# Optimization experiments

Hardware: AMD Instinct MI355X
Metric: run time of the kernel (lower is better)

The kernel has to match this reference:

```python
import jax, jax.numpy as jnp
import numpy as np

# static multi-level geometry (stride 8/16/32/64 on a 1024x1024 image)
SPATIAL_SHAPES = np.array([[128, 128], [64, 64], [32, 32], [16, 16]], dtype=np.int64)
LEVEL_START = np.array([0, 16384, 20480, 21504], dtype=np.int64)
LEN_IN = 21760
N_HEADS, N_LEVELS, N_POINTS = 8, 4, 4
D_MODEL, D_FFN = 256, 1024
N_BATCH, LEN_Q = 8, 2048
EPS = 1e-5


def layer_norm(x, g, b):
    mu = jnp.mean(x, -1, keepdims=True)
    var = jnp.mean((x - mu) ** 2, -1, keepdims=True)
    return (x - mu) * jax.lax.rsqrt(var + EPS) * g + b


def sample_level(val_l, loc_l, Hl, Wl):
    # val_l: [N, nh, Hl*Wl, dh]; loc_l: [N, nh, Lq, P, 2] normalized to [0,1]
    # bilinear, align_corners=False, zero padding (matches F.grid_sample in MSDeformAttn)
    N, nh, _, dh = val_l.shape
    Lq, P = loc_l.shape[2], loc_l.shape[3]
    x = loc_l[..., 0] * Wl - 0.5
    y = loc_l[..., 1] * Hl - 0.5
    x0 = jnp.floor(x)
    y0 = jnp.floor(y)
    wx = (x - x0)[..., None]
    wy = (y - y0)[..., None]

    def gather(xi, yi):
        valid = (xi >= 0) & (xi < Wl) & (yi >= 0) & (yi < Hl)
        xi_c = jnp.clip(xi, 0, Wl - 1).astype(jnp.int32)
        yi_c = jnp.clip(yi, 0, Hl - 1).astype(jnp.int32)
        idx = (yi_c * Wl + xi_c).reshape(N, nh, Lq * P)
        g = jnp.take_along_axis(val_l, idx[..., None], axis=2).reshape(N, nh, Lq, P, dh)
        return g * valid[..., None].astype(val_l.dtype)

    v00 = gather(x0, y0)
    v01 = gather(x0 + 1, y0)
    v10 = gather(x0, y0 + 1)
    v11 = gather(x0 + 1, y0 + 1)
    return v00 * (1 - wx) * (1 - wy) + v01 * wx * (1 - wy) + v10 * (1 - wx) * wy + v11 * wx * wy


def setup_inputs() -> dict:
    key = jax.random.key(0)
    ks = jax.random.split(key, 16)
    s = 0.02
    inp = {
        'src': jax.random.normal(ks[0], (N_BATCH, LEN_Q, D_MODEL), jnp.float32),
        'pos_embed': jax.random.normal(ks[1], (N_BATCH, LEN_Q, D_MODEL), jnp.float32),
        'memorys': jax.random.normal(ks[2], (N_BATCH, LEN_IN, D_MODEL), jnp.float32),
        'pos_memory': jax.random.normal(ks[3], (N_BATCH, LEN_IN, D_MODEL), jnp.float32),
        'reference_points': jax.random.uniform(ks[4], (N_BATCH, LEN_Q, N_LEVELS, 2), jnp.float32),
        'spatial_shapes': jnp.asarray(SPATIAL_SHAPES),
        'level_start_index': jnp.asarray(LEVEL_START),
        # MSDeformAttn params
        'W_off': jax.random.normal(ks[5], (D_MODEL, N_HEADS * N_LEVELS * N_POINTS * 2), jnp.float32) * s,
        'b_off': jax.random.normal(ks[6], (N_HEADS * N_LEVELS * N_POINTS * 2,), jnp.float32) * s,
        'W_attn': jax.random.normal(ks[7], (D_MODEL, N_HEADS * N_LEVELS * N_POINTS), jnp.float32) * s,
        'b_attn': jnp.zeros((N_HEADS * N_LEVELS * N_POINTS,), jnp.float32),
        'W_val': jax.random.normal(ks[8], (D_MODEL, D_MODEL), jnp.float32) * s,
        'b_val': jnp.zeros((D_MODEL,), jnp.float32),
        'W_out': jax.random.normal(ks[9], (D_MODEL, D_MODEL), jnp.float32) * s,
        'b_out': jnp.zeros((D_MODEL,), jnp.float32),
        # norm1
        'g1': jnp.ones((D_MODEL,), jnp.float32),
        'be1': jnp.zeros((D_MODEL,), jnp.float32),
        # FFN (default: linear -> relu -> linear, residual + LayerNorm)
        'W_ff1': jax.random.normal(ks[10], (D_MODEL, D_FFN), jnp.float32) * s,
        'b_ff1': jnp.zeros((D_FFN,), jnp.float32),
        'W_ff2': jax.random.normal(ks[11], (D_FFN, D_MODEL), jnp.float32) * s,
        'b_ff2': jnp.zeros((D_MODEL,), jnp.float32),
        'g2': jnp.ones((D_MODEL,), jnp.float32),
        'be2': jnp.zeros((D_MODEL,), jnp.float32),
    }
    return inp


def reference(src, pos_embed, memorys, pos_memory, reference_points,
              spatial_shapes, level_start_index,
              W_off, b_off, W_attn, b_attn, W_val, b_val, W_out, b_out,
              g1, be1, W_ff1, b_ff1, W_ff2, b_ff2, g2, be2):
    N, Lq, D = src.shape
    nh, L, P = N_HEADS, N_LEVELS, N_POINTS
    dh = D // nh

    q = src + pos_embed                                   # with_pos_embed(src, pos)
    v = (memorys + pos_memory) @ W_val + b_val            # value_proj: [N, Lin, D]
    v = v.reshape(N, -1, nh, dh).transpose(0, 2, 1, 3)    # [N, nh, Lin, dh]

    off = (q @ W_off + b_off).reshape(N, Lq, nh, L, P, 2)
    attn = (q @ W_attn + b_attn).reshape(N, Lq, nh, L * P)
    attn = jax.nn.softmax(attn, axis=-1).reshape(N, Lq, nh, L, P)

    # offset normalizer is (W, H) per level (static geometry)
    norm = jnp.asarray(SPATIAL_SHAPES[:, ::-1].copy(), dtype=src.dtype)
    loc = reference_points[:, :, None, :, None, :] + off / norm[None, None, None, :, None, :]
    loc = loc.transpose(0, 2, 1, 3, 4, 5)                 # [N, nh, Lq, L, P, 2]
    attn = attn.transpose(0, 2, 1, 3, 4)                  # [N, nh, Lq, L, P]

    out = jnp.zeros((N, nh, Lq, dh), src.dtype)
    for l in range(L):  # small static loop over pyramid levels
        Hl, Wl = int(SPATIAL_SHAPES[l, 0]), int(SPATIAL_SHAPES[l, 1])
        s0 = int(LEVEL_START[l])
        val_l = jax.lax.dynamic_slice_in_dim(v, s0, Hl * Wl, axis=2)
        samp = sample_level(val_l, loc[:, :, :, l], Hl, Wl)   # [N, nh, Lq, P, dh]
        out = out + jnp.einsum('nhqp,nhqpd->nhqd', attn[:, :, :, l], samp)

    out = out.transpose(0, 2, 1, 3).reshape(N, Lq, D)
    src2 = out @ W_out + b_out                            # output_proj
    x = layer_norm(src + src2, g1, be1)                   # add + norm1 (dropout=eval identity)
    h = jax.nn.relu(x @ W_ff1 + b_ff1) @ W_ff2 + b_ff2    # default FFN
    return layer_norm(x + h, g2, be2)
```

## Files before the change

kernel.cpp:

```cpp
#include <hip/hip_runtime.h>
#include <hip/hip_bf16.h>
#include <stdint.h>

typedef __attribute__((ext_vector_type(4))) float f32x4;
typedef __attribute__((ext_vector_type(8))) short bf16x8;
typedef __attribute__((ext_vector_type(8))) unsigned short u16x8;
typedef __attribute__((ext_vector_type(4))) unsigned short u16x4;

#define LEN_Q 2048
#define D_MODEL 256
#define LEN_IN 21760

static __device__ __forceinline__ unsigned short f2bf(float f) {
  unsigned int u = __float_as_uint(f);
  u += 0x7fffu + ((u >> 16) & 1u);
  return (unsigned short)(u >> 16);
}
static __device__ __forceinline__ float bf2f(unsigned int us) {
  return __uint_as_float(us << 16);
}

__global__ __launch_bounds__(256) void prep_k(
    const float* __restrict__ Wv, const float* __restrict__ Wo,
    const float* __restrict__ Wa, const float* __restrict__ Wu,
    const float* __restrict__ W1, const float* __restrict__ W2,
    const float* __restrict__ boff, const float* __restrict__ batt,
    unsigned short* __restrict__ WTv, unsigned short* __restrict__ WToa,
    unsigned short* __restrict__ WTu, unsigned short* __restrict__ WT1,
    unsigned short* __restrict__ WT2, float* __restrict__ b_oa) {
  int i = blockIdx.x * 256 + threadIdx.x;
  if (i < 65536) { int n = i >> 8, k = i & 255; WTv[i] = f2bf(Wv[k * 256 + n]); return; }
  i -= 65536;
  if (i < 65536) { int n = i >> 8, k = i & 255; WToa[i] = f2bf(Wo[k * 256 + n]); return; }
  i -= 65536;
  if (i < 32768) { int n = i >> 8, k = i & 255; WToa[65536 + i] = f2bf(Wa[k * 128 + n]); return; }
  i -= 32768;
  if (i < 65536) { int n = i >> 8, k = i & 255; WTu[i] = f2bf(Wu[k * 256 + n]); return; }
  i -= 65536;
  if (i < 262144) { int n = i >> 8, k = i & 255; WT1[i] = f2bf(W1[k * 1024 + n]); return; }
  i -= 262144;
  if (i < 262144) { int n = i >> 10, k = i & 1023; WT2[i] = f2bf(W2[k * 256 + n]); return; }
  i -= 262144;
  if (i < 256) { b_oa[i] = boff[i]; return; }
  i -= 256;
  if (i < 128) { b_oa[256 + i] = batt[i]; }
}

__global__ __launch_bounds__(256) void addcvt_k(const float* __restrict__ a,
                                                const float* __restrict__ b,
                                                unsigned short* __restrict__ o, int n4) {
  int i = blockIdx.x * 256 + threadIdx.x;
  if (i < n4) {
    f32x4 x = ((const f32x4*)a)[i];
    f32x4 y = ((const f32x4*)b)[i];
    u16x4 r;
#pragma unroll
    for (int j = 0; j < 4; ++j) r[j] = f2bf(x[j] + y[j]);
    ((u16x4*)o)[i] = r;
  }
}

template <int FUSEA, int BM, int BN, int EPI>
__global__ __launch_bounds__(512) void gemm2_k(
    const float* __restrict__ A1, const float* __restrict__ A2,
    const unsigned short* __restrict__ Abf,
    const unsigned short* __restrict__ BT, const float* __restrict__ bias,
    float* __restrict__ Of, unsigned short* __restrict__ Ob,
    int M, int N, int K) {
  constexpr int WR = (BM == 128) ? 4 : 2;
  constexpr int WC = 8 / WR;
  constexpr int MR = BM / (16 * WR);
  constexpr int NF = BN / (16 * WC);
  constexpr int ABYTES = BM * 64;
  constexpr int BBYTES = BN * 64;
  __shared__ __align__(128) unsigned short As[2][BM][32];
  __shared__ __align__(128) unsigned short Bs[2][BN][32];

  const int tid = threadIdx.x;
  const int w = tid >> 6, lane = tid & 63;
  const int wr = w / WC, wc = w % WC;
  const int lr = lane & 15, lk = (lane >> 4) << 3;
  const int bm0 = blockIdx.x * BM, bn0 = blockIdx.y * BN;

  f32x4 acc[MR][NF];
#pragma unroll
  for (int m = 0; m < MR; ++m)
#pragma unroll
    for (int g = 0; g < NF; ++g) acc[m][g] = (f32x4){0.f, 0.f, 0.f, 0.f};

  const int srow = lane >> 2;
  const int skb = (lane & 3) << 3;
  auto stage = [&](unsigned short* lbase, const unsigned short* gbase, int kst, int bytes_) {
    for (int off = w * 1024; off < bytes_; off += 8192) {
      const unsigned short* src = gbase + (size_t)((off >> 6) + srow) * kst + skb;
      __builtin_amdgcn_global_load_lds(
          (const __attribute__((address_space(1))) unsigned int*)src,
          (__attribute__((address_space(3))) unsigned int*)((char*)lbase + off),
          16, 0, 0);
    }
  };

  const int arow = tid >> 2;
  const int ak8 = (tid & 3) << 3;
  f32x4 r10, r11, r20, r21;
  auto loadA = [&](int k0) {
    const float* p1 = A1 + (size_t)(bm0 + arow) * K + k0 + ak8;
    const float* p2 = A2 + (size_t)(bm0 + arow) * K + k0 + ak8;
    r10 = *(const f32x4*)p1;
    r11 = *(const f32x4*)(p1 + 4);
    r20 = *(const f32x4*)p2;
    r21 = *(const f32x4*)(p2 + 4);
  };
  auto writeA = [&](int p) {
    u16x8 tv;
#pragma unroll
    for (int j = 0; j < 4; ++j) {
      tv[j] = f2bf(r10[j] + r20[j]);
      tv[4 + j] = f2bf(r11[j] + r21[j]);
    }
    *(u16x8*)&As[p][arow][ak8] = tv;
  };

  const int NT = K >> 5;
  stage(&Bs[0][0][0], BT + (size_t)bn0 * K, K, BBYTES);
  if (FUSEA) {
    loadA(0);
    writeA(0);
  } else {
    stage(&As[0][0][0], Abf + (size_t)bm0 * K, K, ABYTES);
  }
  __syncthreads();

  int p = 0;
  for (int t = 0; t < NT; ++t) {
    const int kn = (t + 1) << 5;
    if (t + 1 < NT) {
      stage(&Bs[p ^ 1][0][0], BT + (size_t)bn0 * K + kn, K, BBYTES);
      if (FUSEA) loadA(kn);
      else stage(&As[p ^ 1][0][0], Abf + (size_t)bm0 * K + kn, K, ABYTES);
    }
    bf16x8 af[MR];
#pragma unroll
    for (int m = 0; m < MR; ++m)
      af[m] = *(const bf16x8*)&As[p][wr * (BM / WR) + m * 16 + lr][lk];
#pragma unroll
    for (int g = 0; g < NF; ++g) {
      bf16x8 bv = *(const bf16x8*)&Bs[p][wc * (BN / WC) + g * 16 + lr][lk];
#pragma unroll
      for (int m = 0; m < MR; ++m)
        acc[m][g] = __builtin_amdgcn_mfma_f32_16x16x32_bf16(af[m], bv, acc[m][g], 0, 0, 0);
    }
    if (FUSEA && t + 1 < NT) writeA(p ^ 1);
    __syncthreads();
    p ^= 1;
  }

#pragma unroll
  for (int m = 0; m < MR; ++m) {
    const int rg = bm0 + wr * (BM / WR) + m * 16 + ((lane >> 4) << 2);
#pragma unroll
    for (int g = 0; g < NF; ++g) {
      const int cg = bn0 + wc * (BN / WC) + g * 16 + lr;
      const float bv = bias[cg];
#pragma unroll
      for (int r = 0; r < 4; ++r) {
        float val = acc[m][g][r] + bv;
        if (EPI == 2) val = fmaxf(val, 0.f);
        size_t o = (size_t)(rg + r) * N + cg;
        if (EPI == 1) Of[o] = val;
        else Ob[o] = f2bf(val);
      }
    }
  }
}

__global__ __launch_bounds__(128) void msda_k(
    const float* __restrict__ offattn, const float* __restrict__ refp,
    const unsigned short* __restrict__ v, unsigned short* __restrict__ out) {
  const int row = blockIdx.x;
  const int n = row >> 11;
  const int t = threadIdx.x;
  const int h = t >> 4, c2 = t & 15;
  const float* oa = offattn + (size_t)row * 384;
  const float* at = oa + 256 + h * 16;
  float lg[16];
  float mx = -1e30f;
#pragma unroll
  for (int i = 0; i < 16; ++i) { lg[i] = at[i]; mx = fmaxf(mx, lg[i]); }
  float den = 0.f;
#pragma unroll
  for (int i = 0; i < 16; ++i) { lg[i] = __expf(lg[i] - mx); den += lg[i]; }
  const float rden = 1.f / den;

  const int HL[4] = {128, 64, 32, 16};
  const int S0[4] = {0, 16384, 20480, 21504};
  float acc0 = 0.f, acc1 = 0.f;
  const unsigned short* vb = v + (size_t)n * LEN_IN * 256 + h * 32 + (c2 << 1);
#pragma unroll
  for (int l = 0; l < 4; ++l) {
    const int W = HL[l], H = HL[l];
    const float Wf = (float)W;
    const int s0 = S0[l];
    const float rx = refp[(size_t)row * 8 + l * 2 + 0];
    const float ry = refp[(size_t)row * 8 + l * 2 + 1];
#pragma unroll
    for (int p = 0; p < 4; ++p) {
      const float ox = oa[h * 32 + l * 8 + p * 2 + 0];
      const float oy = oa[h * 32 + l * 8 + p * 2 + 1];
      float x = rx * Wf + ox - 0.5f;
      float y = ry * Wf + oy - 0.5f;
      float x0f = floorf(x), y0f = floorf(y);
      float wx = x - x0f, wy = y - y0f;
      int x0 = (int)x0f, y0 = (int)y0f;
      float wgt = lg[l * 4 + p] * rden;
#pragma unroll
      for (int cy = 0; cy < 2; ++cy) {
        int yi = y0 + cy;
        float wyf = cy ? wy : (1.f - wy);
        bool vy = (yi >= 0) & (yi < H);
        int yc = min(max(yi, 0), H - 1);
#pragma unroll
        for (int cx = 0; cx < 2; ++cx) {
          int xi = x0 + cx;
          float wxf = cx ? wx : (1.f - wx);
          bool vx = (xi >= 0) & (xi < W);
          int xc = min(max(xi, 0), W - 1);
          unsigned int pv = *(const unsigned int*)(vb + (size_t)(s0 + yc * W + xc) * 256);
          float wv = (vx & vy) ? (wgt * wyf * wxf) : 0.f;
          acc0 += wv * bf2f(pv & 0xffffu);
          acc1 += wv * bf2f(pv >> 16);
        }
      }
    }
  }
  unsigned int pr = ((unsigned int)f2bf(acc1) << 16) | (unsigned int)f2bf(acc0);
  *(unsigned int*)(out + (size_t)row * 256 + h * 32 + (c2 << 1)) = pr;
}

__global__ __launch_bounds__(256) void ln_k(
    const float* __restrict__ resid, const float* __restrict__ y,
    const float* __restrict__ g, const float* __restrict__ b,
    float* __restrict__ Of, unsigned short* __restrict__ Ob) {
  const int row = blockIdx.x, t = threadIdx.x;
  const size_t idx = (size_t)row * 256 + t;
  const float v = resid[idx] + y[idx];
  float s1 = v, s2 = v * v;
#pragma unroll
  for (int d = 32; d > 0; d >>= 1) {
    s1 += __shfl_xor(s1, d, 64);
    s2 += __shfl_xor(s2, d, 64);
  }
  __shared__ float p1[4], p2[4];
  const int w = t >> 6;
  if ((t & 63) == 0) { p1[w] = s1; p2[w] = s2; }
  __syncthreads();
  const float mu = (p1[0] + p1[1] + p1[2] + p1[3]) * (1.f / 256.f);
  const float m2 = (p2[0] + p2[1] + p2[2] + p2[3]) * (1.f / 256.f);
  const float var = m2 - mu * mu;
  const float o = (v - mu) * rsqrtf(var + 1e-5f) * g[t] + b[t];
  Of[idx] = o;
  if (Ob) Ob[idx] = f2bf(o);
}

extern "C" void kernel_launch(void* const* d_in, const int* in_sizes, int n_in,
                              void* d_out, int out_size, void* d_ws, size_t ws_size,
                              hipStream_t stream) {
  const float* src   = (const float*)d_in[0];
  const float* pos   = (const float*)d_in[1];
  const float* mem   = (const float*)d_in[2];
  const float* posm  = (const float*)d_in[3];
  const float* refp  = (const float*)d_in[4];
  const float* W_off = (const float*)d_in[7];
  const float* b_off = (const float*)d_in[8];
  const float* W_at  = (const float*)d_in[9];
  const float* b_at  = (const float*)d_in[10];
  const float* W_val = (const float*)d_in[11];
  const float* b_val = (const float*)d_in[12];
  const float* W_out = (const float*)d_in[13];
  const float* b_out = (const float*)d_in[14];
  const float* g1    = (const float*)d_in[15];
  const float* be1   = (const float*)d_in[16];
  const float* W_ff1 = (const float*)d_in[17];
  const float* b_ff1 = (const float*)d_in[18];
  const float* W_ff2 = (const float*)d_in[19];
  const float* b_ff2 = (const float*)d_in[20];
  const float* g2    = (const float*)d_in[21];
  const float* be2   = (const float*)d_in[22];
  float* out = (float*)d_out;

  const int R = 8 * LEN_Q;
  const int MV = 8 * LEN_IN;

  char* ws = (char*)d_ws;
  size_t woff = 0;
  auto alloc = [&](size_t bytes) {
    char* p = ws + woff;
    woff += (bytes + 255) & ~(size_t)255;
    return p;
  };
  unsigned short* WT_val = (unsigned short*)alloc(256 * 256 * 2);
  unsigned short* WT_oa  = (unsigned short*)alloc(384 * 256 * 2);
  float* b_oa            = (float*)alloc(384 * 4);
  unsigned short* WT_out = (unsigned short*)alloc(256 * 256 * 2);
  unsigned short* WT_f1  = (unsigned short*)alloc(1024 * 256 * 2);
  unsigned short* WT_f2  = (unsigned short*)alloc(256 * 1024 * 2);
  unsigned short* qb     = (unsigned short*)alloc((size_t)R * 256 * 2);
  unsigned short* vb     = (unsigned short*)alloc((size_t)MV * 256 * 2);
  float* offattn         = (float*)alloc((size_t)R * 384 * 4);
  unsigned short* attno  = (unsigned short*)alloc((size_t)R * 256 * 2);
  float* tmp             = (float*)alloc((size_t)R * 256 * 4);
  float* xf              = (float*)alloc((size_t)R * 256 * 4);
  unsigned short* xb     = (unsigned short*)alloc((size_t)R * 256 * 2);
  unsigned short* hb     = (unsigned short*)alloc((size_t)R * 1024 * 2);

  prep_k<<<2946, 256, 0, stream>>>(W_val, W_off, W_at, W_out, W_ff1, W_ff2,
                                   b_off, b_at, WT_val, WT_oa, WT_out, WT_f1,
                                   WT_f2, b_oa);
  addcvt_k<<<4096, 256, 0, stream>>>(src, pos, qb, R * 64);

  gemm2_k<1, 128, 256, 0><<<dim3(MV / 128, 1), 512, 0, stream>>>(
      mem, posm, nullptr, WT_val, b_val, nullptr, vb, MV, 256, 256);
  gemm2_k<0, 64, 128, 1><<<dim3(R / 64, 3), 512, 0, stream>>>(
      nullptr, nullptr, qb, WT_oa, b_oa, offattn, nullptr, R, 384, 256);
  msda_k<<<R, 128, 0, stream>>>(offattn, refp, vb, attno);
  gemm2_k<0, 64, 256, 1><<<dim3(R / 64, 1), 512, 0, stream>>>(
      nullptr, nullptr, attno, WT_out, b_out, tmp, nullptr, R, 256, 256);
  ln_k<<<R, 256, 0, stream>>>(src, tmp, g1, be1, xf, xb);
  gemm2_k<0, 128, 256, 2><<<dim3(R / 128, 4), 512, 0, stream>>>(
      nullptr, nullptr, xb, WT_f1, b_ff1, nullptr, hb, R, 1024, 256);
  gemm2_k<0, 64, 256, 1><<<dim3(R / 64, 1), 512, 0, stream>>>(
      nullptr, nullptr, hb, WT_f2, b_ff2, tmp, nullptr, R, 256, 1024);
  ln_k<<<R, 256, 0, stream>>>(xf, tmp, g2, be2, out, nullptr);
}
```

Before: 609.8 us.

## Keep GEMM weights in registers and use persistent value-projection kernel

Replaces the generic double-buffered GEMM with kernels that hold the whole weight slice for each wave in registers and stage full-K A tiles in XOR-swizzled LDS. The value projection becomes a persistent kernel of 256 blocks, each walking about ten 64-row tiles with a register prefetch of the next tile. The query projection now fuses the src+pos add, which removes the separate add/convert kernel and its buffer. In exchange, register pressure is much higher (the FFN2 variant holds 32 bf16x8 vectors per wave), which risks lower occupancy or spills, and the small grids may leave compute units underused.

```diff
diff --git a/kernel.cpp b/kernel.cpp
--- a/kernel.cpp
+++ b/kernel.cpp
@@ -5,10 +5,8 @@
 typedef __attribute__((ext_vector_type(4))) float f32x4;
 typedef __attribute__((ext_vector_type(8))) short bf16x8;
 typedef __attribute__((ext_vector_type(8))) unsigned short u16x8;
-typedef __attribute__((ext_vector_type(4))) unsigned short u16x4;
 
 #define LEN_Q 2048
-#define D_MODEL 256
 #define LEN_IN 21760
 
 static __device__ __forceinline__ unsigned short f2bf(float f) {
@@ -46,121 +44,191 @@
   if (i < 128) { b_oa[256 + i] = batt[i]; }
 }
 
-__global__ __launch_bounds__(256) void addcvt_k(const float* __restrict__ a,
-                                                const float* __restrict__ b,
-                                                unsigned short* __restrict__ o, int n4) {
-  int i = blockIdx.x * 256 + threadIdx.x;
-  if (i < n4) {
-    f32x4 x = ((const f32x4*)a)[i];
-    f32x4 y = ((const f32x4*)b)[i];
-    u16x4 r;
-#pragma unroll
-    for (int j = 0; j < 4; ++j) r[j] = f2bf(x[j] + y[j]);
-    ((u16x4*)o)[i] = r;
-  }
-}
-
-template <int FUSEA, int BM, int BN, int EPI>
-__global__ __launch_bounds__(512) void gemm2_k(
+__global__ __launch_bounds__(512) void gemmv_k(
+    const float* __restrict__ A1, const float* __restrict__ A2,
+    const unsigned short* __restrict__ BT, const float* __restrict__ bias,
+    unsigned short* __restrict__ Ob) {
+  __shared__ unsigned short As[2][64][256];
+  const int tid = threadIdx.x;
+  const int w = tid >> 6, lane = tid & 63;
+  const int lr = lane & 15, lk8 = (lane >> 4) << 3;
+
+  bf16x8 breg[2][8];
+#pragma unroll
+  for (int g = 0; g < 2; ++g) {
+    const unsigned short* bp = BT + (size_t)(w * 32 + g * 16 + lr) * 256 + lk8;
+#pragma unroll
+    for (int c = 0; c < 8; ++c) breg[g][c] = *(const bf16x8*)(bp + c * 32);
+  }
+  float bv0[2];
+#pragma unroll
+  for (int g = 0; g < 2; ++g) bv0[g] = bias[w * 32 + g * 16 + lr];
+
+  const int b = blockIdx.x;
+  const int nt = 10 + (b < 160 ? 1 : 0);
+  int t = b * 10 + (b < 160 ? b : 160);
+
+  const int row = tid >> 3;
+  const int c0 = (tid & 7) << 5;
+  char* const lbase0 = (char*)&As[0][0][0] + (row << 9);
+  char* const lbase1 = (char*)&As[1][0][0] + (row << 9);
+
+  f32x4 a1[8], a2[8];
+  auto issueA = [&](int tt) {
+    const float* p1 = A1 + (((size_t)(tt * 64 + row)) << 8) + c0;
+    const float* p2 = A2 + (((size_t)(tt * 64 + row)) << 8) + c0;
+#pragma unroll
+    for (int j = 0; j < 8; ++j) {
+      a1[j] = *(const f32x4*)(p1 + j * 4);
+      a2[j] = *(const f32x4*)(p2 + j * 4);
+    }
+  };
+  auto writeA = [&](int buf) {
+    char* base = buf ? lbase1 : lbase0;
+#pragma unroll
+    for (int j = 0; j < 4; ++j) {
+      u16x8 tv;
+#pragma unroll
+      for (int q = 0; q < 4; ++q) {
+        tv[q] = f2bf(a1[2 * j][q] + a2[2 * j][q]);
+        tv[4 + q] = f2bf(a1[2 * j + 1][q] + a2[2 * j + 1][q]);
+      }
+      int off = ((c0 + j * 8) << 1) ^ ((row & 7) << 4);
+      *(u16x8*)(base + off) = tv;
+    }
+  };
+
+  issueA(t);
+  writeA(0);
+  __syncthreads();
+
+  int p = 0;
+  for (int i = 0; i < nt; ++i, ++t) {
+    if (i + 1 < nt) issueA(t + 1);
+    f32x4 acc[4][2];
+#pragma unroll
+    for (int m = 0; m < 4; ++m)
+#pragma unroll
+      for (int g = 0; g < 2; ++g) acc[m][g] = (f32x4){0.f, 0.f, 0.f, 0.f};
+    const char* rb = (const char*)&As[p][0][0];
+#pragma unroll
+    for (int c = 0; c < 8; ++c) {
+      bf16x8 af[4];
+#pragma unroll
+      for (int m = 0; m < 4; ++m) {
+        const int r_ = m * 16 + lr;
+        int off = (r_ << 9) + ((c * 32 + lk8) << 1);
+        off ^= (r_ & 7) << 4;
+        af[m] = *(const bf16x8*)(rb + off);
+      }
+#pragma unroll
+      for (int g = 0; g < 2; ++g)
+#pragma unroll
+        for (int m = 0; m < 4; ++m)
+          acc[m][g] = __builtin_amdgcn_mfma_f32_16x16x32_bf16(af[m], breg[g][c], acc[m][g], 0, 0, 0);
+    }
+#pragma unroll
+    for (int m = 0; m < 4; ++m) {
+      const int rg = t * 64 + m * 16 + ((lane >> 4) << 2);
+#pragma unroll
+      for (int g = 0; g < 2; ++g) {
+        const int cg = w * 32 + g * 16 + lr;
+#pragma unroll
+        for (int r = 0; r < 4; ++r)
+          Ob[((size_t)(rg + r) << 8) + cg] = f2bf(acc[m][g][r] + bv0[g]);
+      }
+    }
+    if (i + 1 < nt) writeA(p ^ 1);
+    __syncthreads();
+    p ^= 1;
+  }
+}
+
+template <int FUSEA, int NF, int KK, int EPI>
+__global__ __launch_bounds__(512) void gemmq_k(
     const float* __restrict__ A1, const float* __restrict__ A2,
     const unsigned short* __restrict__ Abf,
     const unsigned short* __restrict__ BT, const float* __restrict__ bias,
-    float* __restrict__ Of, unsigned short* __restrict__ Ob,
-    int M, int N, int K) {
-  constexpr int WR = (BM == 128) ? 4 : 2;
-  constexpr int WC = 8 / WR;
-  constexpr int MR = BM / (16 * WR);
-  constexpr int NF = BN / (16 * WC);
-  constexpr int ABYTES = BM * 64;
-  constexpr int BBYTES = BN * 64;
-  __shared__ __align__(128) unsigned short As[2][BM][32];
-  __shared__ __align__(128) unsigned short Bs[2][BN][32];
-
+    float* __restrict__ Of, unsigned short* __restrict__ Ob, int N) {
+  constexpr int NSUP = KK / 256;
+  __shared__ unsigned short As[64][256];
   const int tid = threadIdx.x;
   const int w = tid >> 6, lane = tid & 63;
-  const int wr = w / WC, wc = w % WC;
-  const int lr = lane & 15, lk = (lane >> 4) << 3;
-  const int bm0 = blockIdx.x * BM, bn0 = blockIdx.y * BN;
-
-  f32x4 acc[MR][NF];
-#pragma unroll
-  for (int m = 0; m < MR; ++m)
+  const int lr = lane & 15, lk8 = (lane >> 4) << 3;
+  const int bm0 = blockIdx.x * 64, bn0 = blockIdx.y * (NF * 128);
+
+  bf16x8 breg[NF][KK / 32];
+#pragma unroll
+  for (int g = 0; g < NF; ++g) {
+    const unsigned short* bp = BT + (size_t)(bn0 + w * 16 * NF + g * 16 + lr) * KK + lk8;
+#pragma unroll
+    for (int c = 0; c < KK / 32; ++c) breg[g][c] = *(const bf16x8*)(bp + c * 32);
+  }
+
+  f32x4 acc[4][NF];
+#pragma unroll
+  for (int m = 0; m < 4; ++m)
 #pragma unroll
     for (int g = 0; g < NF; ++g) acc[m][g] = (f32x4){0.f, 0.f, 0.f, 0.f};
 
-  const int srow = lane >> 2;
-  const int skb = (lane & 3) << 3;
-  auto stage = [&](unsigned short* lbase, const unsigned short* gbase, int kst, int bytes_) {
-    for (int off = w * 1024; off < bytes_; off += 8192) {
-      const unsigned short* src = gbase + (size_t)((off >> 6) + srow) * kst + skb;
-      __builtin_amdgcn_global_load_lds(
-          (const __attribute__((address_space(1))) unsigned int*)src,
-          (__attribute__((address_space(3))) unsigned int*)((char*)lbase + off),
-          16, 0, 0);
-    }
-  };
-
-  const int arow = tid >> 2;
-  const int ak8 = (tid & 3) << 3;
-  f32x4 r10, r11, r20, r21;
-  auto loadA = [&](int k0) {
-    const float* p1 = A1 + (size_t)(bm0 + arow) * K + k0 + ak8;
-    const float* p2 = A2 + (size_t)(bm0 + arow) * K + k0 + ak8;
-    r10 = *(const f32x4*)p1;
-    r11 = *(const f32x4*)(p1 + 4);
-    r20 = *(const f32x4*)p2;
-    r21 = *(const f32x4*)(p2 + 4);
-  };
-  auto writeA = [&](int p) {
-    u16x8 tv;
-#pragma unroll
-    for (int j = 0; j < 4; ++j) {
-      tv[j] = f2bf(r10[j] + r20[j]);
-      tv[4 + j] = f2bf(r11[j] + r21[j]);
-    }
-    *(u16x8*)&As[p][arow][ak8] = tv;
-  };
-
-  const int NT = K >> 5;
-  stage(&Bs[0][0][0], BT + (size_t)bn0 * K, K, BBYTES);
-  if (FUSEA) {
-    loadA(0);
-    writeA(0);
-  } else {
-    stage(&As[0][0][0], Abf + (size_t)bm0 * K, K, ABYTES);
-  }
-  __syncthreads();
-
-  int p = 0;
-  for (int t = 0; t < NT; ++t) {
-    const int kn = (t + 1) << 5;
-    if (t + 1 < NT) {
-      stage(&Bs[p ^ 1][0][0], BT + (size_t)bn0 * K + kn, K, BBYTES);
-      if (FUSEA) loadA(kn);
-      else stage(&As[p ^ 1][0][0], Abf + (size_t)bm0 * K + kn, K, ABYTES);
-    }
-    bf16x8 af[MR];
-#pragma unroll
-    for (int m = 0; m < MR; ++m)
-      af[m] = *(const bf16x8*)&As[p][wr * (BM / WR) + m * 16 + lr][lk];
+  const int row = tid >> 3, c0 = (tid & 7) << 5;
+  char* const wbase = (char*)&As[0][0] + (row << 9);
+
+#pragma unroll
+  for (int s = 0; s < NSUP; ++s) {
+    if (s) __syncthreads();
+    if (FUSEA) {
+      const float* p1 = A1 + (size_t)(bm0 + row) * KK + s * 256 + c0;
+      const float* p2 = A2 + (size_t)(bm0 + row) * KK + s * 256 + c0;
+#pragma unroll
+      for (int j = 0; j < 4; ++j) {
+        f32x4 u0 = *(const f32x4*)(p1 + j * 8);
+        f32x4 u1 = *(const f32x4*)(p1 + j * 8 + 4);
+        f32x4 v0 = *(const f32x4*)(p2 + j * 8);
+        f32x4 v1 = *(const f32x4*)(p2 + j * 8 + 4);
+        u16x8 tv;
+#pragma unroll
+        for (int q = 0; q < 4; ++q) {
+          tv[q] = f2bf(u0[q] + v0[q]);
+          tv[4 + q] = f2bf(u1[q] + v1[q]);
+        }
+        int off = ((c0 + j * 8) << 1) ^ ((row & 7) << 4);
+        *(u16x8*)(wbase + off) = tv;
+      }
+    } else {
+      const unsigned short* pa = Abf + (size_t)(bm0 + row) * KK + s * 256 + c0;
+#pragma unroll
+      for (int j = 0; j < 4; ++j) {
+        u16x8 tv = *(const u16x8*)(pa + j * 8);
+        int off = ((c0 + j * 8) << 1) ^ ((row & 7) << 4);
+        *(u16x8*)(wbase + off) = tv;
+      }
+    }
+    __syncthreads();
+#pragma unroll
+    for (int c = 0; c < 8; ++c) {
+      bf16x8 af[4];
+#pragma unroll
+      for (int m = 0; m < 4; ++m) {
+        const int r_ = m * 16 + lr;
+        int off = (r_ << 9) + ((c * 32 + lk8) << 1);
+        off ^= (r_ & 7) << 4;
+        af[m] = *(const bf16x8*)((const char*)&As[0][0] + off);
+      }
+#pragma unroll
+      for (int g = 0; g < NF; ++g)
+#pragma unroll
+        for (int m = 0; m < 4; ++m)
+          acc[m][g] = __builtin_amdgcn_mfma_f32_16x16x32_bf16(af[m], breg[g][s * 8 + c], acc[m][g], 0, 0, 0);
+    }
+  }
+
+#pragma unroll
+  for (int m = 0; m < 4; ++m) {
+    const int rg = bm0 + m * 16 + ((lane >> 4) << 2);
 #pragma unroll
     for (int g = 0; g < NF; ++g) {
-      bf16x8 bv = *(const bf16x8*)&Bs[p][wc * (BN / WC) + g * 16 + lr][lk];
-#pragma unroll
-      for (int m = 0; m < MR; ++m)
-        acc[m][g] = __builtin_amdgcn_mfma_f32_16x16x32_bf16(af[m], bv, acc[m][g], 0, 0, 0);
-    }
-    if (FUSEA && t + 1 < NT) writeA(p ^ 1);
-    __syncthreads();
-    p ^= 1;
-  }
-
-#pragma unroll
-  for (int m = 0; m < MR; ++m) {
-    const int rg = bm0 + wr * (BM / WR) + m * 16 + ((lane >> 4) << 2);
-#pragma unroll
-    for (int g = 0; g < NF; ++g) {
-      const int cg = bn0 + wc * (BN / WC) + g * 16 + lr;
+      const int cg = bn0 + w * 16 * NF + g * 16 + lr;
       const float bv = bias[cg];
 #pragma unroll
       for (int r = 0; r < 4; ++r) {
@@ -304,7 +372,6 @@
   unsigned short* WT_out = (unsigned short*)alloc(256 * 256 * 2);
   unsigned short* WT_f1  = (unsigned short*)alloc(1024 * 256 * 2);
   unsigned short* WT_f2  = (unsigned short*)alloc(256 * 1024 * 2);
-  unsigned short* qb     = (unsigned short*)alloc((size_t)R * 256 * 2);
   unsigned short* vb     = (unsigned short*)alloc((size_t)MV * 256 * 2);
   float* offattn         = (float*)alloc((size_t)R * 384 * 4);
   unsigned short* attno  = (unsigned short*)alloc((size_t)R * 256 * 2);
@@ -316,19 +383,21 @@
   prep_k<<<2946, 256, 0, stream>>>(W_val, W_off, W_at, W_out, W_ff1, W_ff2,
                                    b_off, b_at, WT_val, WT_oa, WT_out, WT_f1,
                                    WT_f2, b_oa);
-  addcvt_k<<<4096, 256, 0, stream>>>(src, pos, qb, R * 64);
-
-  gemm2_k<1, 128, 256, 0><<<dim3(MV / 128, 1), 512, 0, stream>>>(
-      mem, posm, nullptr, WT_val, b_val, nullptr, vb, MV, 256, 256);
-  gemm2_k<0, 64, 128, 1><<<dim3(R / 64, 3), 512, 0, stream>>>(
-      nullptr, nullptr, qb, WT_oa, b_oa, offattn, nullptr, R, 384, 256);
+
+  gemmv_k<<<256, 512, 0, stream>>>(mem, posm, WT_val, b_val, vb);
+
+  gemmq_k<1, 3, 256, 1><<<dim3(R / 64, 1), 512, 0, stream>>>(
+      src, pos, nullptr, WT_oa, b_oa, offattn, nullptr, 384);
+
   msda_k<<<R, 128, 0, stream>>>(offattn, refp, vb, attno);
-  gemm2_k<0, 64, 256, 1><<<dim3(R / 64, 1), 512, 0, stream>>>(
-      nullptr, nullptr, attno, WT_out, b_out, tmp, nullptr, R, 256, 256);
+
+  gemmq_k<0, 2, 256, 1><<<dim3(R / 64, 1), 512, 0, stream>>>(
+      nullptr, nullptr, attno, WT_out, b_out, tmp, nullptr, 256);
   ln_k<<<R, 256, 0, stream>>>(src, tmp, g1, be1, xf, xb);
-  gemm2_k<0, 128, 256, 2><<<dim3(R / 128, 4), 512, 0, stream>>>(
-      nullptr, nullptr, xb, WT_f1, b_ff1, nullptr, hb, R, 1024, 256);
-  gemm2_k<0, 64, 256, 1><<<dim3(R / 64, 1), 512, 0, stream>>>(
-      nullptr, nullptr, hb, WT_f2, b_ff2, tmp, nullptr, R, 256, 1024);
+
+  gemmq_k<0, 4, 256, 2><<<dim3(R / 64, 2), 512, 0, stream>>>(
+      nullptr, nullptr, xb, WT_f1, b_ff1, nullptr, hb, 1024);
+  gemmq_k<0, 1, 1024, 1><<<dim3(R / 64, 2), 512, 0, stream>>>(
+      nullptr, nullptr, hb, WT_f2, b_ff2, tmp, nullptr, 256);
   ln_k<<<R, 256, 0, stream>>>(xf, tmp, g2, be2, out, nullptr);
 }
```

Result: no change. 619.8 us (+1.6%).
